# Kernel tuning notes

Hardware: AMD Instinct MI355X
Metric: run time of the kernel (lower is better)

Reference implementation:

```python
import jax, jax.numpy as jnp
import numpy as np

TARGET_W, TARGET_H = 1024, 1024  # cv2 target_size = (width, height)
LANCZOS_A = 4  # cv2.INTER_LANCZOS4 -> 8-tap separable Lanczos, a=4


def _lanczos_matrix(n_in: int, n_out: int) -> jnp.ndarray:
    """Dense [n_out, n_in] separable Lanczos4 resampling matrix.

    OpenCV pixel-center mapping: src = (dst + 0.5) * (n_in / n_out) - 0.5,
    8 taps around floor(src), weights normalized to sum 1, replicate border.
    """
    a = LANCZOS_A
    scale = n_in / n_out
    centers = (jnp.arange(n_out, dtype=jnp.float32) + 0.5) * scale - 0.5
    base = jnp.floor(centers).astype(jnp.int32)
    taps = jnp.arange(-a + 1, a + 1, dtype=jnp.int32)          # [-3..4], 8 taps
    idx = base[:, None] + taps[None, :]                         # [n_out, 8]
    d = centers[:, None] - idx.astype(jnp.float32)
    w = jnp.sinc(d) * jnp.sinc(d / a)                           # lanczos(d)
    w = jnp.where(jnp.abs(d) < a, w, 0.0)
    w = w / jnp.sum(w, axis=1, keepdims=True)
    idx_c = jnp.clip(idx, 0, n_in - 1)                          # replicate border
    rows = jnp.broadcast_to(jnp.arange(n_out)[:, None], idx.shape)
    return jnp.zeros((n_out, n_in), dtype=jnp.float32).at[rows, idx_c].add(w)


def _resize_lanczos4(x: jnp.ndarray, out_h: int, out_w: int) -> jnp.ndarray:
    # x: [B, C, H, W] -> [B, C, out_h, out_w] via two GEMM contractions
    Wh = _lanczos_matrix(x.shape[2], out_h)
    Ww = _lanczos_matrix(x.shape[3], out_w)
    t = jnp.einsum('oh,bchw->bcow', Wh, x)   # resample height: o=out_h
    return jnp.einsum('pw,bcow->bcop', Ww, t)  # resample width: p=out_w


def _renormalize(img: jnp.ndarray) -> jnp.ndarray:
    # Per-image (over C,H,W) range renormalization, faithful to the torch loop.
    mn = jnp.min(img, axis=(1, 2, 3), keepdims=True)
    mx = jnp.max(img, axis=(1, 2, 3), keepdims=True)
    color_range = mx - mn
    ott = jnp.float32(1.0 / 255.0)    # over_top_target_range
    ubt = jnp.float32(-10.0 / 255.0)  # under_bottom_target_range
    otr = mx - 1.0                    # over_top_range
    safe_otr = jnp.where(otr != 0, otr, 1.0)
    v1 = jnp.where(img > 1,
                   (img - 1.0) * (ott / safe_otr) + (1.0 - ott),
                   jnp.where(img < 1, img * (1.0 - ott), img))
    safe_ubr = jnp.where(mn != 0, mn, 1.0)  # under_bottom_range = mn (pre-modification)
    v2 = jnp.where(v1 < 0,
                   v1 * (ubt / safe_ubr) + ubt,
                   jnp.where(v1 > 0, v1 * (1.0 - ubt), v1))
    return jnp.where(color_range > 1, v2, img)


def setup_inputs() -> dict:
    key = jax.random.key(0)
    x = jax.random.normal(key, (32, 3, 512, 512), dtype=jnp.float32)
    return {"x": x}


def reference(x):
    y = _resize_lanczos4(x, TARGET_H, TARGET_W)
    y = _renormalize(y)
    y = y * 255.0
    return y.astype(jnp.uint8)
```

## Files before the change

kernel.cpp:

```cpp
#include <hip/hip_runtime.h>

#define IN_HW 512
#define OUT_HW 1024
#define NB 32
#define NC 3
#define TOH 32
#define TOW 128
#define NTHREADS 256

typedef float  f32x4 __attribute__((ext_vector_type(4)));
typedef int    i32x4 __attribute__((ext_vector_type(4)));

__device__ __forceinline__ unsigned enc_f(float f) {
  unsigned u = __float_as_uint(f);
  return (u & 0x80000000u) ? ~u : (u | 0x80000000u);
}
__device__ __forceinline__ float dec_f(unsigned k) {
  unsigned u = (k & 0x80000000u) ? (k ^ 0x80000000u) : ~k;
  return __uint_as_float(u);
}

#define LW_A -0.00397053f
#define LW_B  0.03146474f
#define LW_C -0.09165979f
#define LW_D  0.28268104f
#define LW_E  0.89337959f
#define LW_F -0.15228947f
#define LW_G  0.05544842f
#define LW_H -0.01505400f

__global__ void k_init(unsigned* __restrict__ maxk, unsigned* __restrict__ mink) {
  int i = threadIdx.x;
  if (i < NB) maxk[i] = 0u;
  else if (i < 2 * NB) mink[i - NB] = 0xFFFFFFFFu;
}

__device__ __forceinline__ void lanczos_tile(
    const float* __restrict__ xchan, int oh0, int ow0, int o, int p,
    float pr2[2][8]) {
  const int row0 = (oh0 >> 1) - 4;
  const int qb = ((ow0 >> 1) - 4) >> 2;

  const float w0[8] = {LW_A, LW_B, LW_C, LW_D, LW_E, LW_F, LW_G, LW_H};
  const float w1[8] = {LW_H, LW_G, LW_F, LW_E, LW_D, LW_C, LW_B, LW_A};

  float ve[12], vo[12];
#pragma unroll
  for (int c = 0; c < 12; ++c) { ve[c] = 0.f; vo[c] = 0.f; }

#pragma unroll
  for (int j = 0; j < 9; ++j) {
    int gr = row0 + p + j;
    gr = gr < 0 ? 0 : (gr > IN_HW - 1 ? IN_HW - 1 : gr);
    const float* __restrict__ rowp = xchan + ((size_t)gr << 9);
#pragma unroll
    for (int g = 0; g < 3; ++g) {
      const int q = qb + o + g;
      const int qc = q < 0 ? 0 : (q > IN_HW / 4 - 1 ? IN_HW / 4 - 1 : q);
      float4 t = reinterpret_cast<const float4*>(rowp)[qc];
      if (q < 0)            { float e = rowp[0];         t = make_float4(e, e, e, e); }
      if (q > IN_HW / 4 - 1){ float e = rowp[IN_HW - 1]; t = make_float4(e, e, e, e); }
      const float tv[4] = {t.x, t.y, t.z, t.w};
#pragma unroll
      for (int c = 0; c < 4; ++c) {
        if (j < 8) ve[4 * g + c] = fmaf(w0[j], tv[c], ve[4 * g + c]);
        if (j > 0) vo[4 * g + c] = fmaf(w1[j - 1], tv[c], vo[4 * g + c]);
      }
    }
  }

#pragma unroll
  for (int row = 0; row < 2; ++row) {
    const float* v = row ? vo : ve;
#pragma unroll
    for (int m = 0; m < 4; ++m) {
      float pe = 0.f, po = 0.f;
#pragma unroll
      for (int j = 0; j < 8; ++j) {
        pe = fmaf(w0[j], v[m + j], pe);
        po = fmaf(w1[j], v[m + 1 + j], po);
      }
      pr2[row][2 * m] = pe; pr2[row][2 * m + 1] = po;
    }
  }
}

__global__ __launch_bounds__(NTHREADS) void k_resize(
    const float* __restrict__ x, float* __restrict__ outf,
    unsigned* __restrict__ maxk, unsigned* __restrict__ mink) {
  __shared__ float wred[8];
  const int tid = threadIdx.x;
  const int bc = blockIdx.z;
  const int oh0 = blockIdx.y * TOH, ow0 = blockIdx.x * TOW;
  const float* __restrict__ xchan = x + (size_t)bc * (IN_HW * IN_HW);
  const int o = tid & 15;
  const int p = tid >> 4;
  float pr2[2][8];
  lanczos_tile(xchan, oh0, ow0, o, p, pr2);

  const size_t base = (size_t)bc * (OUT_HW * OUT_HW) +
                      (size_t)(oh0 + 2 * p) * OUT_HW + (ow0 + 8 * o);
#pragma unroll
  for (int row = 0; row < 2; ++row) {
    float* dst = outf + base + (size_t)row * OUT_HW;
    *reinterpret_cast<float4*>(dst)     = make_float4(pr2[row][0], pr2[row][1],
                                                      pr2[row][2], pr2[row][3]);
    *reinterpret_cast<float4*>(dst + 4) = make_float4(pr2[row][4], pr2[row][5],
                                                      pr2[row][6], pr2[row][7]);
  }

  float mx = pr2[0][0], mn = pr2[0][0];
#pragma unroll
  for (int r = 0; r < 2; ++r)
#pragma unroll
    for (int i = 0; i < 8; ++i) {
      mx = fmaxf(mx, pr2[r][i]); mn = fminf(mn, pr2[r][i]);
    }
#pragma unroll
  for (int s = 32; s > 0; s >>= 1) {
    mx = fmaxf(mx, __shfl_xor(mx, s, 64));
    mn = fminf(mn, __shfl_xor(mn, s, 64));
  }
  if ((tid & 63) == 0) { wred[tid >> 6] = mx; wred[4 + (tid >> 6)] = mn; }
  __syncthreads();
  if (tid == 0) {
    float bmx = fmaxf(fmaxf(wred[0], wred[1]), fmaxf(wred[2], wred[3]));
    float bmn = fminf(fminf(wred[4], wred[5]), fminf(wred[6], wred[7]));
    int b = bc / NC;
    atomicMax(&maxk[b], enc_f(bmx));
    atomicMin(&mink[b], enc_f(bmn));
  }
}

__device__ __forceinline__ int renorm1(float img, bool applies, float cA, float cB,
                                       float om_ott, float om_ubt) {
  const float ott = 1.0f / 255.0f;
  const float ubt = -10.0f / 255.0f;
  float v1 = (img > 1.0f) ? fmaf(img - 1.0f, cA, 1.0f - ott)
           : (img < 1.0f) ? img * om_ott : img;
  float v2 = (v1 < 0.0f) ? fmaf(v1, cB, ubt)
           : (v1 > 0.0f) ? v1 * om_ubt : v1;
  float y = (applies ? v2 : img) * 255.0f;
  int t = (int)y;
  return t < 0 ? 0 : (t > 255 ? 255 : t);
}

#define N4_PER_IMG (NC * OUT_HW * OUT_HW / 4)

__global__ __launch_bounds__(NTHREADS) void k_renorm(
    int* out, const unsigned* __restrict__ maxk, const unsigned* __restrict__ mink) {
  const int b = blockIdx.y;
  const float mx = dec_f(maxk[b]);
  const float mn = dec_f(mink[b]);
  const bool applies = (mx - mn) > 1.0f;
  const float ott = 1.0f / 255.0f;
  const float ubt = -10.0f / 255.0f;
  const float otr = mx - 1.0f;
  const float cA = ott / ((otr != 0.0f) ? otr : 1.0f);
  const float cB = ubt / ((mn != 0.0f) ? mn : 1.0f);
  const float om_ott = 1.0f - ott;
  const float om_ubt = 1.0f - ubt;

  const size_t idx = (size_t)b * N4_PER_IMG +
                     (size_t)blockIdx.x * NTHREADS + threadIdx.x;
  const f32x4 v = __builtin_nontemporal_load(
      reinterpret_cast<const f32x4*>(out) + idx);
  i32x4 r;
  r.x = renorm1(v.x, applies, cA, cB, om_ott, om_ubt);
  r.y = renorm1(v.y, applies, cA, cB, om_ott, om_ubt);
  r.z = renorm1(v.z, applies, cA, cB, om_ott, om_ubt);
  r.w = renorm1(v.w, applies, cA, cB, om_ott, om_ubt);
  __builtin_nontemporal_store(r, reinterpret_cast<i32x4*>(out) + idx);
}

extern "C" void kernel_launch(void* const* d_in, const int* in_sizes, int n_in,
                              void* d_out, int out_size, void* d_ws, size_t ws_size,
                              hipStream_t stream) {
  const float* x = (const float*)d_in[0];
  unsigned* maxk = (unsigned*)d_ws;
  unsigned* mink = maxk + NB;

  hipLaunchKernelGGL(k_init, dim3(1), dim3(64), 0, stream, maxk, mink);
  dim3 grid(OUT_HW / TOW, OUT_HW / TOH, NB * NC);
  hipLaunchKernelGGL(k_resize, grid, dim3(NTHREADS), 0, stream,
                     x, (float*)d_out, maxk, mink);
  hipLaunchKernelGGL(k_renorm, dim3(N4_PER_IMG / NTHREADS, NB), dim3(NTHREADS),
                     0, stream, (int*)d_out, maxk, mink);
}
```

Before: 774.2 us.

## Compute four output rows per thread and add unclamped interior fast path

```diff
diff --git a/kernel.cpp b/kernel.cpp
--- a/kernel.cpp
+++ b/kernel.cpp
@@ -4,7 +4,7 @@
 #define OUT_HW 1024
 #define NB 32
 #define NC 3
-#define TOH 32
+#define TOH 64
 #define TOW 128
 #define NTHREADS 256
 
@@ -35,57 +35,33 @@
   else if (i < 2 * NB) mink[i - NB] = 0xFFFFFFFFu;
 }
 
-__device__ __forceinline__ void lanczos_tile(
-    const float* __restrict__ xchan, int oh0, int ow0, int o, int p,
-    float pr2[2][8]) {
-  const int row0 = (oh0 >> 1) - 4;
-  const int qb = ((ow0 >> 1) - 4) >> 2;
-
-  const float w0[8] = {LW_A, LW_B, LW_C, LW_D, LW_E, LW_F, LW_G, LW_H};
-  const float w1[8] = {LW_H, LW_G, LW_F, LW_E, LW_D, LW_C, LW_B, LW_A};
-
-  float ve[12], vo[12];
-#pragma unroll
-  for (int c = 0; c < 12; ++c) { ve[c] = 0.f; vo[c] = 0.f; }
-
-#pragma unroll
-  for (int j = 0; j < 9; ++j) {
-    int gr = row0 + p + j;
-    gr = gr < 0 ? 0 : (gr > IN_HW - 1 ? IN_HW - 1 : gr);
-    const float* __restrict__ rowp = xchan + ((size_t)gr << 9);
-#pragma unroll
-    for (int g = 0; g < 3; ++g) {
-      const int q = qb + o + g;
-      const int qc = q < 0 ? 0 : (q > IN_HW / 4 - 1 ? IN_HW / 4 - 1 : q);
-      float4 t = reinterpret_cast<const float4*>(rowp)[qc];
-      if (q < 0)            { float e = rowp[0];         t = make_float4(e, e, e, e); }
-      if (q > IN_HW / 4 - 1){ float e = rowp[IN_HW - 1]; t = make_float4(e, e, e, e); }
-      const float tv[4] = {t.x, t.y, t.z, t.w};
-#pragma unroll
-      for (int c = 0; c < 4; ++c) {
-        if (j < 8) ve[4 * g + c] = fmaf(w0[j], tv[c], ve[4 * g + c]);
-        if (j > 0) vo[4 * g + c] = fmaf(w1[j - 1], tv[c], vo[4 * g + c]);
-      }
+__device__ __forceinline__ void vert_accum(
+    const float tv[12], int j, const float w0[8], const float w1[8],
+    float vAe[12], float vAo[12], float vBe[12], float vBo[12]) {
+#pragma unroll
+  for (int c = 0; c < 12; ++c) {
+    if (j < 8)           vAe[c] = fmaf(w0[j],     tv[c], vAe[c]);
+    if (j >= 1 && j < 9) vAo[c] = fmaf(w1[j - 1], tv[c], vAo[c]);
+    if (j >= 1 && j < 9) vBe[c] = fmaf(w0[j - 1], tv[c], vBe[c]);
+    if (j >= 2)          vBo[c] = fmaf(w1[j - 2], tv[c], vBo[c]);
+  }
+}
+
+__device__ __forceinline__ void horiz8(
+    const float v[12], const float w0[8], const float w1[8], float px[8]) {
+#pragma unroll
+  for (int m = 0; m < 4; ++m) {
+    float pe = 0.f, po = 0.f;
+#pragma unroll
+    for (int j = 0; j < 8; ++j) {
+      pe = fmaf(w0[j], v[m + j], pe);
+      po = fmaf(w1[j], v[m + 1 + j], po);
     }
-  }
-
-#pragma unroll
-  for (int row = 0; row < 2; ++row) {
-    const float* v = row ? vo : ve;
-#pragma unroll
-    for (int m = 0; m < 4; ++m) {
-      float pe = 0.f, po = 0.f;
-#pragma unroll
-      for (int j = 0; j < 8; ++j) {
-        pe = fmaf(w0[j], v[m + j], pe);
-        po = fmaf(w1[j], v[m + 1 + j], po);
-      }
-      pr2[row][2 * m] = pe; pr2[row][2 * m + 1] = po;
-    }
-  }
-}
-
-__global__ __launch_bounds__(NTHREADS) void k_resize(
+    px[2 * m] = pe; px[2 * m + 1] = po;
+  }
+}
+
+__global__ __launch_bounds__(NTHREADS, 4) void k_resize(
     const float* __restrict__ x, float* __restrict__ outf,
     unsigned* __restrict__ maxk, unsigned* __restrict__ mink) {
   __shared__ float wred[8];
@@ -95,27 +71,67 @@
   const float* __restrict__ xchan = x + (size_t)bc * (IN_HW * IN_HW);
   const int o = tid & 15;
   const int p = tid >> 4;
-  float pr2[2][8];
-  lanczos_tile(xchan, oh0, ow0, o, p, pr2);
+  const int k = (oh0 >> 1) + 2 * p;
+  const int rowbase = k - 4;
+  const int qb = ((ow0 >> 1) - 4) >> 2;
+  const int q0 = qb + o;
+
+  const float w0[8] = {LW_A, LW_B, LW_C, LW_D, LW_E, LW_F, LW_G, LW_H};
+  const float w1[8] = {LW_H, LW_G, LW_F, LW_E, LW_D, LW_C, LW_B, LW_A};
+
+  float vAe[12], vAo[12], vBe[12], vBo[12];
+#pragma unroll
+  for (int c = 0; c < 12; ++c) { vAe[c] = vAo[c] = vBe[c] = vBo[c] = 0.f; }
+
+  const bool fast = (blockIdx.x > 0) & (blockIdx.x < 7) &
+                    (blockIdx.y > 0) & (blockIdx.y < (OUT_HW / TOH) - 1);
+  if (fast) {
+    const float* __restrict__ tp = xchan + (size_t)rowbase * IN_HW + 4 * q0;
+#pragma unroll
+    for (int j = 0; j < 10; ++j) {
+      const f32x4 a = *reinterpret_cast<const f32x4*>(tp + (size_t)j * IN_HW);
+      const f32x4 b = *reinterpret_cast<const f32x4*>(tp + (size_t)j * IN_HW + 4);
+      const f32x4 c = *reinterpret_cast<const f32x4*>(tp + (size_t)j * IN_HW + 8);
+      const float tv[12] = {a.x, a.y, a.z, a.w, b.x, b.y, b.z, b.w,
+                            c.x, c.y, c.z, c.w};
+      vert_accum(tv, j, w0, w1, vAe, vAo, vBe, vBo);
+    }
+  } else {
+#pragma unroll
+    for (int j = 0; j < 10; ++j) {
+      int gr = rowbase + j;
+      gr = gr < 0 ? 0 : (gr > IN_HW - 1 ? IN_HW - 1 : gr);
+      const float* __restrict__ rowp = xchan + ((size_t)gr << 9);
+      float tv[12];
+#pragma unroll
+      for (int g = 0; g < 3; ++g) {
+        const int q = q0 + g;
+        const int qc = q < 0 ? 0 : (q > IN_HW / 4 - 1 ? IN_HW / 4 - 1 : q);
+        f32x4 v = reinterpret_cast<const f32x4*>(rowp)[qc];
+        if (q < 0)             { float e = rowp[0];         v = (f32x4){e, e, e, e}; }
+        if (q > IN_HW / 4 - 1) { float e = rowp[IN_HW - 1]; v = (f32x4){e, e, e, e}; }
+        tv[4 * g + 0] = v.x; tv[4 * g + 1] = v.y;
+        tv[4 * g + 2] = v.z; tv[4 * g + 3] = v.w;
+      }
+      vert_accum(tv, j, w0, w1, vAe, vAo, vBe, vBo);
+    }
+  }
 
   const size_t base = (size_t)bc * (OUT_HW * OUT_HW) +
-                      (size_t)(oh0 + 2 * p) * OUT_HW + (ow0 + 8 * o);
-#pragma unroll
-  for (int row = 0; row < 2; ++row) {
-    float* dst = outf + base + (size_t)row * OUT_HW;
-    *reinterpret_cast<float4*>(dst)     = make_float4(pr2[row][0], pr2[row][1],
-                                                      pr2[row][2], pr2[row][3]);
-    *reinterpret_cast<float4*>(dst + 4) = make_float4(pr2[row][4], pr2[row][5],
-                                                      pr2[row][6], pr2[row][7]);
-  }
-
-  float mx = pr2[0][0], mn = pr2[0][0];
-#pragma unroll
-  for (int r = 0; r < 2; ++r)
-#pragma unroll
-    for (int i = 0; i < 8; ++i) {
-      mx = fmaxf(mx, pr2[r][i]); mn = fminf(mn, pr2[r][i]);
-    }
+                      (size_t)(oh0 + 4 * p) * OUT_HW + (ow0 + 8 * o);
+  float mx = -__builtin_inff(), mn = __builtin_inff();
+#pragma unroll
+  for (int r = 0; r < 4; ++r) {
+    const float* v = (r == 0) ? vAe : (r == 1) ? vAo : (r == 2) ? vBe : vBo;
+    float px[8];
+    horiz8(v, w0, w1, px);
+#pragma unroll
+    for (int i = 0; i < 8; ++i) { mx = fmaxf(mx, px[i]); mn = fminf(mn, px[i]); }
+    float* dst = outf + base + (size_t)r * OUT_HW;
+    *reinterpret_cast<f32x4*>(dst)     = (f32x4){px[0], px[1], px[2], px[3]};
+    *reinterpret_cast<f32x4*>(dst + 4) = (f32x4){px[4], px[5], px[6], px[7]};
+  }
+
 #pragma unroll
   for (int s = 32; s > 0; s >>= 1) {
     mx = fmaxf(mx, __shfl_xor(mx, s, 64));
@@ -170,7 +186,7 @@
   r.y = renorm1(v.y, applies, cA, cB, om_ott, om_ubt);
   r.z = renorm1(v.z, applies, cA, cB, om_ott, om_ubt);
   r.w = renorm1(v.w, applies, cA, cB, om_ott, om_ubt);
-  __builtin_nontemporal_store(r, reinterpret_cast<i32x4*>(out) + idx);
+  reinterpret_cast<i32x4*>(out)[idx] = r;
 }
 
 extern "C" void kernel_launch(void* const* d_in, const int* in_sizes, int n_in,
```

Measured after the change: 831.4 us. +7.4%, slower.
